# Kernel tuning notes

Hardware: AMD Instinct MI355X
Metric: run time of the kernel (lower is better)

The kernel has to match this reference:

```python
import jax, jax.numpy as jnp
import numpy as np

N_NODES = 21
N_ACTIONS = 256
NODE_FEAT = 128


def _gcn_norm(edge_index, n):
    # Dense normalized adjacency mirroring PyG gcn_norm with add_self_loops=True.
    row, col = edge_index[0], edge_index[1]
    A = jnp.zeros((n, n), dtype=jnp.float32).at[row, col].add(1.0)
    A = A + jnp.eye(n, dtype=jnp.float32)  # self loops appended with weight 1
    deg = A.sum(axis=0)                    # scatter-add of edge weights by col
    dinv = jnp.where(deg > 0, 1.0 / jnp.sqrt(deg), 0.0)
    # out[row] += dinv[row] * dinv[col] * x[col]  ->  A_norm = D^-1/2 A D^-1/2
    return dinv[:, None] * A * dinv[None, :]


def setup_inputs() -> dict:
    key = jax.random.key(0)
    ks = jax.random.split(key, 12)
    B = 65536
    state = jax.random.normal(ks[0], (B, N_NODES, NODE_FEAT), dtype=jnp.float32)
    edge_index = jax.random.randint(ks[1], (2, 128), 0, N_NODES, dtype=jnp.int32)

    def lin(k, fan_in, fan_out):
        s = 1.0 / np.sqrt(fan_in)
        kw, kb = jax.random.split(k)
        W = jax.random.uniform(kw, (fan_in, fan_out), jnp.float32, -s, s)
        b = jax.random.uniform(kb, (fan_out,), jnp.float32, -s, s)
        return W, b

    W1, b1 = lin(ks[2], NODE_FEAT, 21)
    W2, b2 = lin(ks[3], 21, 21)
    Wf1, bf1 = lin(ks[4], 441, 512)
    Wf2, bf2 = lin(ks[5], 512, 512)
    Wf3, bf3 = lin(ks[6], 512, N_ACTIONS)
    return {"state": state, "edge_index": edge_index,
            "W1": W1, "b1": b1, "W2": W2, "b2": b2,
            "Wf1": Wf1, "bf1": bf1, "Wf2": Wf2, "bf2": bf2,
            "Wf3": Wf3, "bf3": bf3}


def reference(state, edge_index, W1, b1, W2, b2, Wf1, bf1, Wf2, bf2, Wf3, bf3):
    A = _gcn_norm(edge_index, N_NODES)                      # [21, 21]
    # GCNConv 1: A_norm @ (X W1) + b1   (no nonlinearity between GCN layers)
    h = jnp.einsum('bnf,fh->bnh', state, W1)                # [B, 21, 21]
    h = jnp.einsum('ij,bjh->bih', A, h) + b1
    # GCNConv 2
    h = jnp.einsum('bnf,fh->bnh', h, W2)
    h = jnp.einsum('ij,bjh->bih', A, h) + b2                # [B, 21, 21]
    v = h.reshape(h.shape[0], -1)[0]                        # x.view(B,-1)[0] -> [441]
    x = jax.nn.relu(v @ Wf1 + bf1)
    x = jax.nn.relu(x @ Wf2 + bf2)
    x = jax.nn.relu(x @ Wf3 + bf3)                          # [n_actions]
    return x
```

## Files before the change

### kernel.cpp

```cpp
#include <hip/hip_runtime.h>
#include <math.h>

#define N_NODES 21
#define NODE_FEAT 128
#define APAD 28
#define W1PAD 132

#define WS_ACC1 0
#define WS_ACC2 512
#define WS_ACC3 1024

__device__ unsigned g_arrive[64 * 16];
__device__ unsigned g_go;
__device__ unsigned g_cnt;

__device__ __forceinline__ float agent_load(const float* p) {
    return __hip_atomic_load(p, __ATOMIC_RELAXED, __HIP_MEMORY_SCOPE_AGENT);
}
__device__ __forceinline__ void agent_store(float* p, float v) {
    __hip_atomic_store(p, v, __ATOMIC_RELAXED, __HIP_MEMORY_SCOPE_AGENT);
}
__device__ __forceinline__ unsigned flag_load(const unsigned* p) {
    return __hip_atomic_load(p, __ATOMIC_RELAXED, __HIP_MEMORY_SCOPE_AGENT);
}
__device__ __forceinline__ void flag_store(unsigned* p, unsigned v) {
    __hip_atomic_store(p, v, __ATOMIC_RELAXED, __HIP_MEMORY_SCOPE_AGENT);
}
__device__ __forceinline__ float agent_fadd(float* p, float v) {
    return __hip_atomic_fetch_add(p, v, __ATOMIC_RELAXED, __HIP_MEMORY_SCOPE_AGENT);
}

__device__ __forceinline__ void lds_barrier() {
    asm volatile("s_waitcnt lgkmcnt(0)\n\ts_barrier" ::: "memory");
}

__device__ __forceinline__ void grid_barrier(int blk, unsigned base, unsigned phase) {
    const unsigned target = base + phase;
    __syncthreads();
    if (blk == 0) {
        if (threadIdx.x > 0 && threadIdx.x < 64) {
            for (;;) {
                unsigned f = flag_load(&g_arrive[threadIdx.x * 16]);
                if ((int)(f - target) >= 0) break;
                __builtin_amdgcn_s_sleep(1);
            }
        }
        if (threadIdx.x == 0) flag_store(&g_go, target);
    } else {
        if (threadIdx.x == 0) {
            flag_store(&g_arrive[blk * 16], target);
            for (;;) {
                unsigned f = flag_load(&g_go);
                if ((int)(f - target) >= 0) break;
                __builtin_amdgcn_s_sleep(1);
            }
        }
    }
    __syncthreads();
}

__global__ __launch_bounds__(512) void fused_kernel(
    const float* __restrict__ state,
    const int*   __restrict__ edge_index,
    const float* __restrict__ W1,
    const float* __restrict__ b1,
    const float* __restrict__ W2,
    const float* __restrict__ b2,
    const float* __restrict__ Wf1,
    const float* __restrict__ bf1,
    const float* __restrict__ Wf2,
    const float* __restrict__ bf2,
    const float* __restrict__ Wf3,
    const float* __restrict__ bf3,
    float* __restrict__ ws,
    float* __restrict__ out)
{
    const int b = blockIdx.x;
    const int t = threadIdx.x;

    const unsigned bbase = flag_load(&g_go);
    const unsigned cbase = flag_load(&g_cnt);

    const bool do_fc1 = (b < 21);
    const bool do_fc2 = (b >= 21 && b < 53);
    const bool do_fc3 = (b < 32);

    __shared__ float sA[21 * APAD];
    __shared__ float sX[21 * W1PAD];
    __shared__ float sW1T[21 * W1PAD];
    __shared__ float sW2T[21 * APAD];
    __shared__ float sT[21 * APAD];
    __shared__ float sG[21 * APAD];
    __shared__ float sv[441];
    __shared__ float sdeg[21];
    __shared__ float sb1[21], sb2[21];
    __shared__ float x1s[16], x2s[16];
    __shared__ unsigned sflag;

    for (int i = t; i < 21 * APAD; i += 512) {
        sA[i] = 0.0f; sW2T[i] = 0.0f; sT[i] = 0.0f; sG[i] = 0.0f;
    }
    if (t < 21) { sdeg[t] = 1.0f; sb1[t] = b1[t]; sb2[t] = b2[t]; }
    {
        const float4* src4 = (const float4*)state;
        for (int i = t; i < 672; i += 512) {
            int n = i >> 5, fc = i & 31;
            ((float4*)&sX[n * W1PAD])[fc] = src4[i];
        }
    }
    for (int i = t; i < 2688; i += 512) {
        int f = i / 21, k = i - f * 21;
        sW1T[k * W1PAD + f] = W1[i];
    }
    for (int i = t; i < 441; i += 512) {
        int f = i / 21, k = i - f * 21;
        sW2T[k * APAD + f] = W2[i];
    }
    int er = 0, ec = 0;
    if (t < 128) { er = edge_index[t]; ec = edge_index[128 + t]; }

    float wf1v[21];
    if (do_fc1) {
        #pragma unroll
        for (int i = 0; i < 21; ++i) wf1v[i] = Wf1[(size_t)(21 * b + i) * 512 + t];
    }
    float wf2v[16];
    float rbf1 = 0.0f;
    if (do_fc2) {
        #pragma unroll
        for (int i = 0; i < 16; ++i) wf2v[i] = Wf2[(size_t)(16 * (b - 21) + i) * 512 + t];
        if (t < 16) rbf1 = bf1[16 * (b - 21) + t];
    }
    float wf3v[16];
    float rbf2 = 0.0f;
    if (do_fc3) {
        if (t < 256) {
            #pragma unroll
            for (int i = 0; i < 16; ++i) wf3v[i] = Wf3[(size_t)(16 * b + i) * 256 + t];
        }
        if (t < 16) rbf2 = bf2[16 * b + t];
    }
    const float rbf3 = bf3[t & 255];

    if (b == 0) {
        agent_store(&ws[WS_ACC1 + t], 0.0f);
        agent_store(&ws[WS_ACC2 + t], 0.0f);
        if (t < 256) agent_store(&ws[WS_ACC3 + t], 0.0f);
    }

    if (b == 0) __syncthreads(); else lds_barrier();
    if (b == 0 && t == 0) flag_store(&g_go, bbase + 1);

    if (t < 128) {
        atomicAdd(&sA[er * APAD + ec], 1.0f);
        atomicAdd(&sdeg[ec], 1.0f);
    }
    if (t < 21) atomicAdd(&sA[t * APAD + t], 1.0f);
    if (t < 441) {
        int n = t / 21, k = t - n * 21;
        const float4* x4 = (const float4*)&sX[n * W1PAD];
        const float4* w4 = (const float4*)&sW1T[k * W1PAD];
        float s = 0.0f;
        #pragma unroll
        for (int fc = 0; fc < 32; ++fc) {
            float4 a = x4[fc], ww = w4[fc];
            s += a.x * ww.x; s += a.y * ww.y; s += a.z * ww.z; s += a.w * ww.w;
        }
        sT[k * APAD + n] = s;
    }
    lds_barrier();

    if (t < 441) {
        int r = t / 21, c = t - r * 21;
        float dr = 1.0f / sqrtf(sdeg[r]);
        float dc = 1.0f / sqrtf(sdeg[c]);
        sA[r * APAD + c] = dr * sA[r * APAD + c] * dc;
    }
    lds_barrier();

    if (t < 441) {
        int r = t / 21, k = t - r * 21;
        const float4* a4 = (const float4*)&sA[r * APAD];
        const float4* h4 = (const float4*)&sT[k * APAD];
        float s = sb1[k];
        #pragma unroll
        for (int jc = 0; jc < 6; ++jc) {
            float4 a = a4[jc], h = h4[jc];
            s += a.x * h.x; s += a.y * h.y; s += a.z * h.z; s += a.w * h.w;
        }
        sG[r * APAD + k] = s;
    }
    lds_barrier();

    if (t < 441) {
        int n = t / 21, k = t - n * 21;
        const float4* g4 = (const float4*)&sG[n * APAD];
        const float4* w4 = (const float4*)&sW2T[k * APAD];
        float s = 0.0f;
        #pragma unroll
        for (int jc = 0; jc < 6; ++jc) {
            float4 g = g4[jc], ww = w4[jc];
            s += g.x * ww.x; s += g.y * ww.y; s += g.z * ww.z; s += g.w * ww.w;
        }
        sT[k * APAD + n] = s;
    }
    lds_barrier();

    if (t < 441) {
        int r = t / 21, k = t - r * 21;
        const float4* a4 = (const float4*)&sA[r * APAD];
        const float4* h4 = (const float4*)&sT[k * APAD];
        float s = sb2[k];
        #pragma unroll
        for (int jc = 0; jc < 6; ++jc) {
            float4 a = a4[jc], h = h4[jc];
            s += a.x * h.x; s += a.y * h.y; s += a.z * h.z; s += a.w * h.w;
        }
        sv[t] = s;
    }
    lds_barrier();

    if (t == 0) {
        while ((int)(flag_load(&g_go) - (bbase + 1)) < 0)
            __builtin_amdgcn_s_sleep(1);
    }
    __syncthreads();

    if (do_fc1) {
        float s = 0.0f;
        #pragma unroll
        for (int r = 0; r < 21; ++r) s += sv[21 * b + r] * wf1v[r];
        agent_fadd(&ws[WS_ACC1 + t], s);
    }

    grid_barrier(b, bbase, 2);

    if (do_fc2) {
        if (t < 16)
            x1s[t] = fmaxf(agent_load(&ws[WS_ACC1 + 16 * (b - 21) + t]) + rbf1, 0.0f);
        lds_barrier();
        float s = 0.0f;
        #pragma unroll
        for (int j = 0; j < 16; ++j) s += x1s[j] * wf2v[j];
        agent_fadd(&ws[WS_ACC2 + t], s);
    }

    grid_barrier(b, bbase, 3);

    if (do_fc3) {
        if (t < 16)
            x2s[t] = fmaxf(agent_load(&ws[WS_ACC2 + 16 * b + t]) + rbf2, 0.0f);
        lds_barrier();
        if (t < 256) {
            float s = 0.0f;
            #pragma unroll
            for (int j = 0; j < 16; ++j) s += x2s[j] * wf3v[j];
            agent_fadd(&ws[WS_ACC3 + t], s);
        }
    }

    __syncthreads();
    if (t == 0) {
        unsigned prev = __hip_atomic_fetch_add(&g_cnt, 1u, __ATOMIC_RELAXED,
                                               __HIP_MEMORY_SCOPE_AGENT);
        sflag = (prev == cbase + 63u) ? 1u : 0u;
    }
    __syncthreads();
    if (sflag && t < 256) {
        float a = agent_load(&ws[WS_ACC3 + t]) + rbf3;
        out[t] = fmaxf(a, 0.0f);
    }
}

extern "C" void kernel_launch(void* const* d_in, const int* in_sizes, int n_in,
                              void* d_out, int out_size, void* d_ws, size_t ws_size,
                              hipStream_t stream)
{
    const float* state      = (const float*)d_in[0];
    const int*   edge_index = (const int*)  d_in[1];
    const float* W1  = (const float*)d_in[2];
    const float* b1  = (const float*)d_in[3];
    const float* W2  = (const float*)d_in[4];
    const float* b2  = (const float*)d_in[5];
    const float* Wf1 = (const float*)d_in[6];
    const float* bf1 = (const float*)d_in[7];
    const float* Wf2 = (const float*)d_in[8];
    const float* bf2 = (const float*)d_in[9];
    const float* Wf3 = (const float*)d_in[10];
    const float* bf3 = (const float*)d_in[11];

    float* ws  = (float*)d_ws;
    float* out = (float*)d_out;

    fused_kernel<<<64, 512, 0, stream>>>(state, edge_index, W1, b1, W2, b2,
                                         Wf1, bf1, Wf2, bf2, Wf3, bf3, ws, out);
}
```

Before: 16.38 us.

## Restrict GCN to FC1 blocks and rebalance FC2/FC3 work across disjoint blocks

Only the 21 FC1 blocks now compute the GCN prologue, so the other blocks skip the shared-memory setup and small matmuls and can reach the grid barriers sooner. FC2 moves to 16 blocks of 32 rows and FC3 to 8 blocks of 64 rows, placed on blocks separate from the GCN ones, with more weights preloaded into registers per block. The grid-barrier bookkeeping switches from epoch-relative counters to absolute phases that the last block resets at the end of each launch. A separate zero-ready flag replaces the initial go signal. The trade-off is higher register pressure and a dependence on the reset running correctly every launch.

```diff
diff --git a/kernel.cpp b/kernel.cpp
--- a/kernel.cpp
+++ b/kernel.cpp
@@ -1,8 +1,6 @@
 #include <hip/hip_runtime.h>
 #include <math.h>
 
-#define N_NODES 21
-#define NODE_FEAT 128
 #define APAD 28
 #define W1PAD 132
 
@@ -12,6 +10,7 @@
 
 __device__ unsigned g_arrive[64 * 16];
 __device__ unsigned g_go;
+__device__ unsigned g_zr;
 __device__ unsigned g_cnt;
 
 __device__ __forceinline__ float agent_load(const float* p) {
@@ -34,26 +33,19 @@
     asm volatile("s_waitcnt lgkmcnt(0)\n\ts_barrier" ::: "memory");
 }
 
-__device__ __forceinline__ void grid_barrier(int blk, unsigned base, unsigned phase) {
-    const unsigned target = base + phase;
+__device__ __forceinline__ void grid_barrier(int blk, unsigned phase) {
     __syncthreads();
     if (blk == 0) {
         if (threadIdx.x > 0 && threadIdx.x < 64) {
-            for (;;) {
-                unsigned f = flag_load(&g_arrive[threadIdx.x * 16]);
-                if ((int)(f - target) >= 0) break;
+            while (flag_load(&g_arrive[threadIdx.x * 16]) < phase)
                 __builtin_amdgcn_s_sleep(1);
-            }
-        }
-        if (threadIdx.x == 0) flag_store(&g_go, target);
+        }
+        if (threadIdx.x == 0) flag_store(&g_go, phase);
     } else {
         if (threadIdx.x == 0) {
-            flag_store(&g_arrive[blk * 16], target);
-            for (;;) {
-                unsigned f = flag_load(&g_go);
-                if ((int)(f - target) >= 0) break;
+            flag_store(&g_arrive[blk * 16], phase);
+            while (flag_load(&g_go) < phase)
                 __builtin_amdgcn_s_sleep(1);
-            }
         }
     }
     __syncthreads();
@@ -78,12 +70,9 @@
     const int b = blockIdx.x;
     const int t = threadIdx.x;
 
-    const unsigned bbase = flag_load(&g_go);
-    const unsigned cbase = flag_load(&g_cnt);
-
-    const bool do_fc1 = (b < 21);
-    const bool do_fc2 = (b >= 21 && b < 53);
-    const bool do_fc3 = (b < 32);
+    const bool is_gcn = (b < 21);
+    const bool do_fc2 = (b >= 21 && b < 37);
+    const bool do_fc3 = (b >= 37 && b < 45);
 
     __shared__ float sA[21 * APAD];
     __shared__ float sX[21 * W1PAD];
@@ -94,167 +83,168 @@
     __shared__ float sv[441];
     __shared__ float sdeg[21];
     __shared__ float sb1[21], sb2[21];
-    __shared__ float x1s[16], x2s[16];
+    __shared__ float x1s[32], x2s[64];
     __shared__ unsigned sflag;
 
-    for (int i = t; i < 21 * APAD; i += 512) {
-        sA[i] = 0.0f; sW2T[i] = 0.0f; sT[i] = 0.0f; sG[i] = 0.0f;
-    }
-    if (t < 21) { sdeg[t] = 1.0f; sb1[t] = b1[t]; sb2[t] = b2[t]; }
-    {
-        const float4* src4 = (const float4*)state;
-        for (int i = t; i < 672; i += 512) {
-            int n = i >> 5, fc = i & 31;
-            ((float4*)&sX[n * W1PAD])[fc] = src4[i];
-        }
-    }
-    for (int i = t; i < 2688; i += 512) {
-        int f = i / 21, k = i - f * 21;
-        sW1T[k * W1PAD + f] = W1[i];
-    }
-    for (int i = t; i < 441; i += 512) {
-        int f = i / 21, k = i - f * 21;
-        sW2T[k * APAD + f] = W2[i];
-    }
-    int er = 0, ec = 0;
-    if (t < 128) { er = edge_index[t]; ec = edge_index[128 + t]; }
-
     float wf1v[21];
-    if (do_fc1) {
+    if (is_gcn) {
         #pragma unroll
         for (int i = 0; i < 21; ++i) wf1v[i] = Wf1[(size_t)(21 * b + i) * 512 + t];
     }
-    float wf2v[16];
+    float wf2v[32];
     float rbf1 = 0.0f;
     if (do_fc2) {
         #pragma unroll
-        for (int i = 0; i < 16; ++i) wf2v[i] = Wf2[(size_t)(16 * (b - 21) + i) * 512 + t];
-        if (t < 16) rbf1 = bf1[16 * (b - 21) + t];
-    }
-    float wf3v[16];
+        for (int i = 0; i < 32; ++i) wf2v[i] = Wf2[(size_t)(32 * (b - 21) + i) * 512 + t];
+        if (t < 32) rbf1 = bf1[32 * (b - 21) + t];
+    }
+    float wf3v[64];
     float rbf2 = 0.0f;
     if (do_fc3) {
         if (t < 256) {
             #pragma unroll
-            for (int i = 0; i < 16; ++i) wf3v[i] = Wf3[(size_t)(16 * b + i) * 256 + t];
-        }
-        if (t < 16) rbf2 = bf2[16 * b + t];
+            for (int i = 0; i < 64; ++i) wf3v[i] = Wf3[(size_t)(64 * (b - 37) + i) * 256 + t];
+        }
+        if (t < 64) rbf2 = bf2[64 * (b - 37) + t];
     }
     const float rbf3 = bf3[t & 255];
 
-    if (b == 0) {
+    if (b == 63) {
         agent_store(&ws[WS_ACC1 + t], 0.0f);
         agent_store(&ws[WS_ACC2 + t], 0.0f);
         if (t < 256) agent_store(&ws[WS_ACC3 + t], 0.0f);
-    }
-
-    if (b == 0) __syncthreads(); else lds_barrier();
-    if (b == 0 && t == 0) flag_store(&g_go, bbase + 1);
-
-    if (t < 128) {
-        atomicAdd(&sA[er * APAD + ec], 1.0f);
-        atomicAdd(&sdeg[ec], 1.0f);
-    }
-    if (t < 21) atomicAdd(&sA[t * APAD + t], 1.0f);
-    if (t < 441) {
-        int n = t / 21, k = t - n * 21;
-        const float4* x4 = (const float4*)&sX[n * W1PAD];
-        const float4* w4 = (const float4*)&sW1T[k * W1PAD];
+        __syncthreads();
+        if (t == 0) flag_store(&g_zr, 1u);
+    }
+
+    if (is_gcn) {
+        for (int i = t; i < 21 * APAD; i += 512) {
+            sA[i] = 0.0f; sW2T[i] = 0.0f; sT[i] = 0.0f; sG[i] = 0.0f;
+        }
+        if (t < 21) { sdeg[t] = 1.0f; sb1[t] = b1[t]; sb2[t] = b2[t]; }
+        {
+            const float4* src4 = (const float4*)state;
+            for (int i = t; i < 672; i += 512) {
+                int n = i >> 5, fc = i & 31;
+                ((float4*)&sX[n * W1PAD])[fc] = src4[i];
+            }
+        }
+        for (int i = t; i < 2688; i += 512) {
+            int f = i / 21, k = i - f * 21;
+            sW1T[k * W1PAD + f] = W1[i];
+        }
+        for (int i = t; i < 441; i += 512) {
+            int f = i / 21, k = i - f * 21;
+            sW2T[k * APAD + f] = W2[i];
+        }
+        int er = 0, ec = 0;
+        if (t < 128) { er = edge_index[t]; ec = edge_index[128 + t]; }
+        lds_barrier();
+
+        if (t < 128) {
+            atomicAdd(&sA[er * APAD + ec], 1.0f);
+            atomicAdd(&sdeg[ec], 1.0f);
+        }
+        if (t < 21) atomicAdd(&sA[t * APAD + t], 1.0f);
+        if (t < 441) {
+            int n = t / 21, k = t - n * 21;
+            const float4* x4 = (const float4*)&sX[n * W1PAD];
+            const float4* w4 = (const float4*)&sW1T[k * W1PAD];
+            float s = 0.0f;
+            #pragma unroll
+            for (int fc = 0; fc < 32; ++fc) {
+                float4 a = x4[fc], ww = w4[fc];
+                s += a.x * ww.x; s += a.y * ww.y; s += a.z * ww.z; s += a.w * ww.w;
+            }
+            sT[k * APAD + n] = s;
+        }
+        lds_barrier();
+
+        if (t < 441) {
+            int r = t / 21, c = t - r * 21;
+            float dr = 1.0f / sqrtf(sdeg[r]);
+            float dc = 1.0f / sqrtf(sdeg[c]);
+            sA[r * APAD + c] = dr * sA[r * APAD + c] * dc;
+        }
+        lds_barrier();
+
+        if (t < 441) {
+            int r = t / 21, k = t - r * 21;
+            const float4* a4 = (const float4*)&sA[r * APAD];
+            const float4* h4 = (const float4*)&sT[k * APAD];
+            float s = sb1[k];
+            #pragma unroll
+            for (int jc = 0; jc < 6; ++jc) {
+                float4 a = a4[jc], h = h4[jc];
+                s += a.x * h.x; s += a.y * h.y; s += a.z * h.z; s += a.w * h.w;
+            }
+            sG[r * APAD + k] = s;
+        }
+        lds_barrier();
+
+        if (t < 441) {
+            int n = t / 21, k = t - n * 21;
+            const float4* g4 = (const float4*)&sG[n * APAD];
+            const float4* w4 = (const float4*)&sW2T[k * APAD];
+            float s = 0.0f;
+            #pragma unroll
+            for (int jc = 0; jc < 6; ++jc) {
+                float4 g = g4[jc], ww = w4[jc];
+                s += g.x * ww.x; s += g.y * ww.y; s += g.z * ww.z; s += g.w * ww.w;
+            }
+            sT[k * APAD + n] = s;
+        }
+        lds_barrier();
+
+        if (t < 441) {
+            int r = t / 21, k = t - r * 21;
+            const float4* a4 = (const float4*)&sA[r * APAD];
+            const float4* h4 = (const float4*)&sT[k * APAD];
+            float s = sb2[k];
+            #pragma unroll
+            for (int jc = 0; jc < 6; ++jc) {
+                float4 a = a4[jc], h = h4[jc];
+                s += a.x * h.x; s += a.y * h.y; s += a.z * h.z; s += a.w * h.w;
+            }
+            sv[t] = s;
+        }
+        lds_barrier();
+
+        if (t == 0) {
+            while (flag_load(&g_zr) == 0u) __builtin_amdgcn_s_sleep(1);
+        }
+        __syncthreads();
+
+        {
+            float s = 0.0f;
+            #pragma unroll
+            for (int r = 0; r < 21; ++r) s += sv[21 * b + r] * wf1v[r];
+            agent_fadd(&ws[WS_ACC1 + t], s);
+        }
+    }
+
+    grid_barrier(b, 1);
+
+    if (do_fc2) {
+        if (t < 32)
+            x1s[t] = fmaxf(agent_load(&ws[WS_ACC1 + 32 * (b - 21) + t]) + rbf1, 0.0f);
+        lds_barrier();
         float s = 0.0f;
         #pragma unroll
-        for (int fc = 0; fc < 32; ++fc) {
-            float4 a = x4[fc], ww = w4[fc];
-            s += a.x * ww.x; s += a.y * ww.y; s += a.z * ww.z; s += a.w * ww.w;
-        }
-        sT[k * APAD + n] = s;
-    }
-    lds_barrier();
-
-    if (t < 441) {
-        int r = t / 21, c = t - r * 21;
-        float dr = 1.0f / sqrtf(sdeg[r]);
-        float dc = 1.0f / sqrtf(sdeg[c]);
-        sA[r * APAD + c] = dr * sA[r * APAD + c] * dc;
-    }
-    lds_barrier();
-
-    if (t < 441) {
-        int r = t / 21, k = t - r * 21;
-        const float4* a4 = (const float4*)&sA[r * APAD];
-        const float4* h4 = (const float4*)&sT[k * APAD];
-        float s = sb1[k];
-        #pragma unroll
-        for (int jc = 0; jc < 6; ++jc) {
-            float4 a = a4[jc], h = h4[jc];
-            s += a.x * h.x; s += a.y * h.y; s += a.z * h.z; s += a.w * h.w;
-        }
-        sG[r * APAD + k] = s;
-    }
-    lds_barrier();
-
-    if (t < 441) {
-        int n = t / 21, k = t - n * 21;
-        const float4* g4 = (const float4*)&sG[n * APAD];
-        const float4* w4 = (const float4*)&sW2T[k * APAD];
-        float s = 0.0f;
-        #pragma unroll
-        for (int jc = 0; jc < 6; ++jc) {
-            float4 g = g4[jc], ww = w4[jc];
-            s += g.x * ww.x; s += g.y * ww.y; s += g.z * ww.z; s += g.w * ww.w;
-        }
-        sT[k * APAD + n] = s;
-    }
-    lds_barrier();
-
-    if (t < 441) {
-        int r = t / 21, k = t - r * 21;
-        const float4* a4 = (const float4*)&sA[r * APAD];
-        const float4* h4 = (const float4*)&sT[k * APAD];
-        float s = sb2[k];
-        #pragma unroll
-        for (int jc = 0; jc < 6; ++jc) {
-            float4 a = a4[jc], h = h4[jc];
-            s += a.x * h.x; s += a.y * h.y; s += a.z * h.z; s += a.w * h.w;
-        }
-        sv[t] = s;
-    }
-    lds_barrier();
-
-    if (t == 0) {
-        while ((int)(flag_load(&g_go) - (bbase + 1)) < 0)
-            __builtin_amdgcn_s_sleep(1);
-    }
-    __syncthreads();
-
-    if (do_fc1) {
-        float s = 0.0f;
-        #pragma unroll
-        for (int r = 0; r < 21; ++r) s += sv[21 * b + r] * wf1v[r];
-        agent_fadd(&ws[WS_ACC1 + t], s);
-    }
-
-    grid_barrier(b, bbase, 2);
-
-    if (do_fc2) {
-        if (t < 16)
-            x1s[t] = fmaxf(agent_load(&ws[WS_ACC1 + 16 * (b - 21) + t]) + rbf1, 0.0f);
-        lds_barrier();
-        float s = 0.0f;
-        #pragma unroll
-        for (int j = 0; j < 16; ++j) s += x1s[j] * wf2v[j];
+        for (int j = 0; j < 32; ++j) s += x1s[j] * wf2v[j];
         agent_fadd(&ws[WS_ACC2 + t], s);
     }
 
-    grid_barrier(b, bbase, 3);
+    grid_barrier(b, 2);
 
     if (do_fc3) {
-        if (t < 16)
-            x2s[t] = fmaxf(agent_load(&ws[WS_ACC2 + 16 * b + t]) + rbf2, 0.0f);
+        if (t < 64)
+            x2s[t] = fmaxf(agent_load(&ws[WS_ACC2 + 64 * (b - 37) + t]) + rbf2, 0.0f);
         lds_barrier();
         if (t < 256) {
             float s = 0.0f;
             #pragma unroll
-            for (int j = 0; j < 16; ++j) s += x2s[j] * wf3v[j];
+            for (int j = 0; j < 64; ++j) s += x2s[j] * wf3v[j];
             agent_fadd(&ws[WS_ACC3 + t], s);
         }
     }
@@ -263,12 +253,18 @@
     if (t == 0) {
         unsigned prev = __hip_atomic_fetch_add(&g_cnt, 1u, __ATOMIC_RELAXED,
                                                __HIP_MEMORY_SCOPE_AGENT);
-        sflag = (prev == cbase + 63u) ? 1u : 0u;
-    }
-    __syncthreads();
-    if (sflag && t < 256) {
-        float a = agent_load(&ws[WS_ACC3 + t]) + rbf3;
-        out[t] = fmaxf(a, 0.0f);
+        sflag = (prev == 63u) ? 1u : 0u;
+    }
+    __syncthreads();
+    if (sflag) {
+        if (t < 256) {
+            float a = agent_load(&ws[WS_ACC3 + t]) + rbf3;
+            out[t] = fmaxf(a, 0.0f);
+        }
+        if (t >= 256 && t < 320) flag_store(&g_arrive[(t - 256) * 16], 0u);
+        if (t == 320) flag_store(&g_go, 0u);
+        if (t == 321) flag_store(&g_zr, 0u);
+        if (t == 322) flag_store(&g_cnt, 0u);
     }
 }
 
```

After: 16.32 us, median of 2. About the same (-0.4%).
